# Optimization experiments

Measured on AMD Instinct MI355X. Metric: run time of the kernel, lower is better.

Reference implementation:

```python
import jax, jax.numpy as jnp
import numpy as np
from jax import lax

B, L, D, C = 4096, 50, 128, 64
V = 100000
H = D // 2  # bidirectional LSTM hidden size; 2*H == emb_dim


def setup_inputs() -> dict:
    key = jax.random.key(0)
    ks = jax.random.split(key, 26)
    f = lambda k, s: jax.random.normal(k, s, dtype=jnp.float32) * 0.05
    return {
        "r_idx": jax.random.randint(ks[0], (B,), 0, V),
        "a_idx": jax.random.randint(ks[1], (B,), 0, V),
        "acc_idx": jax.random.randint(ks[2], (B,), 0, V),
        "rank_q": jax.random.normal(ks[3], (B, L, D), dtype=jnp.float32),
        "rank_q_len": jax.random.randint(ks[4], (B,), 0, L),
        "ru_emb": f(ks[5], (V, D)),
        "au_emb": f(ks[6], (V, D)),
        "Wih_f": f(ks[7], (4 * H, D)), "Whh_f": f(ks[8], (4 * H, H)),
        "bih_f": f(ks[9], (4 * H,)), "bhh_f": f(ks[10], (4 * H,)),
        "Wih_b": f(ks[11], (4 * H, D)), "Whh_b": f(ks[12], (4 * H, H)),
        "bih_b": f(ks[13], (4 * H,)), "bhh_b": f(ks[14], (4 * H,)),
        "conv1_w": f(ks[15], (C, 1, D)), "conv1_b": f(ks[16], (C,)),
        "conv2_w": f(ks[17], (C, 2, D)), "conv2_b": f(ks[18], (C,)),
        "conv3_w": f(ks[19], (C, 3, D)), "conv3_b": f(ks[20], (C,)),
        "fc1_w": f(ks[21], (6,)), "fc1_b": f(ks[22], (1,)),
        "fc2_w": f(ks[23], (C,)), "fc2_b": f(ks[24], (1,)),
    }


def _lstm_dir(x, Wih, Whh, bih, bhh, reverse):
    # x: [B, L, D] -> outputs [B, L, H]; PyTorch gate order i,f,g,o
    b = x.shape[0]
    xs = jnp.swapaxes(x, 0, 1)  # [L, B, D]
    h0 = jnp.zeros((b, Whh.shape[1]), x.dtype)

    def step(carry, xt):
        h, c = carry
        gates = xt @ Wih.T + h @ Whh.T + (bih + bhh)
        i, fg, g, o = jnp.split(gates, 4, axis=-1)
        i = jax.nn.sigmoid(i)
        fg = jax.nn.sigmoid(fg)
        g = jnp.tanh(g)
        o = jax.nn.sigmoid(o)
        c = fg * c + i * g
        h = o * jnp.tanh(c)
        return (h, c), h

    _, ys = lax.scan(step, (h0, h0), xs, reverse=reverse)
    return jnp.swapaxes(ys, 0, 1)


def _score(mat, conv1_w, conv1_b, conv2_w, conv2_b, conv3_w, conv3_b, fc1_w, fc1_b, fc2_w, fc2_b):
    # mat: [B, 3, D]; three tiny conv branches (kernel heights 1/2/3, width=D)
    branches = []
    for w, bias in ((conv1_w, conv1_b), (conv2_w, conv2_b), (conv3_w, conv3_b)):
        k = w.shape[1]
        wins = jnp.stack([mat[:, i:i + k] for i in range(3 - k + 1)], axis=1)  # [B, W, k, D]
        branches.append(jax.nn.relu(jnp.einsum('bwkd,ckd->bcw', wins, w) + bias[None, :, None]))
    s = jnp.concatenate(branches, axis=2)  # [B, C, 6]
    h = jnp.einsum('bcw,w->bc', s, fc1_w) + fc1_b[0]  # fc_new_1: 6 -> 1
    return jnp.einsum('bc,c->b', h, fc2_w) + fc2_b[0]  # fc_new_2: C -> 1


def reference(r_idx, a_idx, acc_idx, rank_q, rank_q_len, ru_emb, au_emb,
              Wih_f, Whh_f, bih_f, bhh_f, Wih_b, Whh_b, bih_b, bhh_b,
              conv1_w, conv1_b, conv2_w, conv2_b, conv3_w, conv3_b,
              fc1_w, fc1_b, fc2_w, fc2_b):
    emb_r = ru_emb[r_idx]
    emb_a = au_emb[a_idx]
    emb_acc = au_emb[acc_idx]
    # bidirectional LSTM over the question sequence
    out_f = _lstm_dir(rank_q, Wih_f, Whh_f, bih_f, bhh_f, reverse=False)
    out_b = _lstm_dir(rank_q, Wih_b, Whh_b, bih_b, bhh_b, reverse=True)
    q_out = jnp.concatenate([out_f, out_b], axis=-1)  # [B, L, D]
    # prepend a zero timestep, then gather per-example at index rank_q_len
    q_pad = jnp.concatenate([jnp.zeros((q_out.shape[0], 1, q_out.shape[2]), q_out.dtype), q_out], axis=1)
    emb_q = q_pad[jnp.arange(q_pad.shape[0]), rank_q_len]  # [B, D]
    low = jnp.stack([emb_r, emb_q, emb_a], axis=1)   # [B, 3, D]
    high = jnp.stack([emb_r, emb_q, emb_acc], axis=1)
    fcp = (conv1_w, conv1_b, conv2_w, conv2_b, conv3_w, conv3_b, fc1_w, fc1_b, fc2_w, fc2_b)
    low_s = _score(low, *fcp)
    high_s = _score(high, *fcp)
    return jnp.sum(low_s - high_s)
```

## Files before the change

kernel.cpp:

```cpp
#include <hip/hip_runtime.h>
#include <hip/hip_bf16.h>

#define LSEQ 50
#define BATCH 4096

typedef __attribute__((ext_vector_type(8))) short bf16x8;
typedef __attribute__((ext_vector_type(4))) float f32x4;

__device__ __forceinline__ unsigned cvtpk(float lo, float hi) {
    unsigned r;
    asm("v_cvt_pk_bf16_f32 %0, %1, %2" : "=v"(r) : "v"(lo), "v"(hi));
    return r;
}
__device__ __forceinline__ bf16x8 pack8(float4 a, float4 b) {
    uint4 u;
    u.x = cvtpk(a.x, a.y); u.y = cvtpk(a.z, a.w);
    u.z = cvtpk(b.x, b.y); u.w = cvtpk(b.z, b.w);
    return __builtin_bit_cast(bf16x8, u);
}
__device__ __forceinline__ float fsigm(float x) {
    return __builtin_amdgcn_rcpf(1.0f + __builtin_amdgcn_exp2f(-1.44269504f * x));
}
__device__ __forceinline__ float ftanh(float x) {
    float e = __builtin_amdgcn_exp2f(2.88539008f * x);
    return 1.0f - 2.0f * __builtin_amdgcn_rcpf(e + 1.0f);
}

__global__ __launch_bounds__(256)
void sort_kernel(const int* __restrict__ qlen, int* __restrict__ perm)
{
    __shared__ int base[64];
    const int tid = threadIdx.x;
    if (tid < 64) base[tid] = 0;
    __syncthreads();
    for (int i = tid; i < BATCH; i += 256) atomicAdd(&base[qlen[i]], 1);
    __syncthreads();
    if (tid == 0) {
        int s = 0;
        for (int v = 0; v < 50; ++v) { int c = base[v]; base[v] = s; s += c; }
    }
    __syncthreads();
    for (int i = tid; i < BATCH; i += 256) {
        int pos = atomicAdd(&base[qlen[i]], 1);
        perm[pos] = i;
    }
}

__global__ __launch_bounds__(256, 2)
void lstm_kernel(const float* __restrict__ rank_q, const int* __restrict__ qlen,
                 const int* __restrict__ perm,
                 const float* __restrict__ Wih_f, const float* __restrict__ Whh_f,
                 const float* __restrict__ bih_f, const float* __restrict__ bhh_f,
                 const float* __restrict__ Wih_b, const float* __restrict__ Whh_b,
                 const float* __restrict__ bih_b, const float* __restrict__ bhh_b,
                 float* __restrict__ embq)
{
    const int blk = blockIdx.x;
    const int dir = blk >> 8;
    const int bb  = blk & 255;
    const int grp = (bb & 1) ? (255 - (bb >> 1)) : (bb >> 1);
    const int b0  = grp << 4;
    const int tid = threadIdx.x;
    const int wv  = tid >> 6;
    const int ln  = tid & 63;
    const int lm  = ln & 15;
    const int lq  = ln >> 4;
    const int m   = (wv << 4) + lm;

    const float* Wih = dir ? Wih_b : Wih_f;
    const float* Whh = dir ? Whh_b : Whh_f;
    const float* bih = dir ? bih_b : bih_f;
    const float* bhh = dir ? bhh_b : bhh_f;

    __shared__ __align__(16) unsigned short xbuf[3][16][136];
    __shared__ __align__(16) unsigned short hbuf[2][16][72];
    __shared__ int len_s[16];

    if (tid < 16) len_s[tid] = qlen[perm[b0 + tid]];
    for (int i = tid; i < 16 * 72; i += 256) ((unsigned short*)hbuf)[i] = 0;

    bf16x8 bfrag[4][6];
    float bias[4];
    #pragma unroll
    for (int j = 0; j < 4; ++j) {
        const int n = (j << 6) + m;
        bias[j] = bih[n] + bhh[n];
        #pragma unroll
        for (int s = 0; s < 6; ++s) {
            const int kb = (s << 5) + (lq << 3);
            const float* src = (s < 4) ? (Wih + n * 128 + kb)
                                       : (Whh + n * 64 + (kb - 128));
            bfrag[j][s] = pack8(*(const float4*)src, *(const float4*)(src + 4));
        }
    }

    int exq[4], len_e[4];
    #pragma unroll
    for (int r = 0; r < 4; ++r) {
        exq[r]   = perm[b0 + (lq << 2) + r];
        len_e[r] = qlen[exq[r]];
    }

    float cst[4]  = {0.f, 0.f, 0.f, 0.f};
    float qval[4] = {0.f, 0.f, 0.f, 0.f};

    const int se  = tid >> 4;
    const int exs = perm[b0 + se];
    const int sd  = (tid & 15) << 3;
    const int tstep = dir ? -128 : 128;
    const float* gp = rank_q + ((size_t)exs * LSEQ + (dir ? LSEQ - 1 : 0)) * 128 + sd;

    __syncthreads();

    int steps;
    if (dir == 0) {
        int mx = 0;
        #pragma unroll
        for (int i = 0; i < 16; ++i) mx = max(mx, len_s[i]);
        steps = mx;
    } else {
        int mn = 51;
        #pragma unroll
        for (int i = 0; i < 16; ++i) { int l = len_s[i]; mn = min(mn, l ? l : 51); }
        steps = (mn == 51) ? 0 : 51 - mn;
    }

    if (steps > 0) {
        {
            float4 a0 = *(const float4*)gp, b0v = *(const float4*)(gp + 4); gp += tstep;
            float4 a1 = *(const float4*)gp, b1v = *(const float4*)(gp + 4); gp += tstep;
            *(bf16x8*)&xbuf[0][se][sd] = pack8(a0, b0v);
            *(bf16x8*)&xbuf[1][se][sd] = pack8(a1, b1v);
        }
        float4 ha, hb2;
        if (3 <= steps) { ha = *(const float4*)gp; hb2 = *(const float4*)(gp + 4); gp += tstep; }
        __syncthreads();

        const int xoff = lm * 136 + (lq << 3);
        const int hoff = lm * 72 + (lq << 3);

        f32x4 accx[4];
        {
            const unsigned short* xb = &xbuf[0][0][0];
            bf16x8 x0 = *(const bf16x8*)(xb + xoff);
            bf16x8 x1 = *(const bf16x8*)(xb + xoff + 32);
            bf16x8 x2 = *(const bf16x8*)(xb + xoff + 64);
            bf16x8 x3 = *(const bf16x8*)(xb + xoff + 96);
            #pragma unroll
            for (int j = 0; j < 4; ++j) {
                f32x4 a = {bias[j], bias[j], bias[j], bias[j]};
                a = __builtin_amdgcn_mfma_f32_16x16x32_bf16(x0, bfrag[j][0], a, 0, 0, 0);
                a = __builtin_amdgcn_mfma_f32_16x16x32_bf16(x1, bfrag[j][1], a, 0, 0, 0);
                a = __builtin_amdgcn_mfma_f32_16x16x32_bf16(x2, bfrag[j][2], a, 0, 0, 0);
                a = __builtin_amdgcn_mfma_f32_16x16x32_bf16(x3, bfrag[j][3], a, 0, 0, 0);
                accx[j] = a;
            }
        }

        int r1 = 1, w2 = 2;
        for (int it = 0; it < steps; ++it) {
            const int t   = dir ? (LSEQ - 1 - it) : it;
            const int rbh = it & 1;
            const int wbh = rbh ^ 1;

            float4 na, nb;
            const bool nv = (it + 4 <= steps);
            if (nv) { na = *(const float4*)gp; nb = *(const float4*)(gp + 4); gp += tstep; }

            const unsigned short* hb = &hbuf[rbh][0][0];
            bf16x8 ah0 = *(const bf16x8*)(hb + hoff);
            bf16x8 ah1 = *(const bf16x8*)(hb + hoff + 32);
            f32x4 gate[4];
            #pragma unroll
            for (int j = 0; j < 4; ++j) {
                f32x4 a = __builtin_amdgcn_mfma_f32_16x16x32_bf16(ah0, bfrag[j][4], accx[j], 0, 0, 0);
                gate[j]  = __builtin_amdgcn_mfma_f32_16x16x32_bf16(ah1, bfrag[j][5], a, 0, 0, 0);
            }

            if (it + 1 < steps) {
                const unsigned short* xb = &xbuf[r1][0][0];
                bf16x8 x0 = *(const bf16x8*)(xb + xoff);
                bf16x8 x1 = *(const bf16x8*)(xb + xoff + 32);
                bf16x8 x2 = *(const bf16x8*)(xb + xoff + 64);
                bf16x8 x3 = *(const bf16x8*)(xb + xoff + 96);
                #pragma unroll
                for (int j = 0; j < 4; ++j) {
                    f32x4 a = {bias[j], bias[j], bias[j], bias[j]};
                    a = __builtin_amdgcn_mfma_f32_16x16x32_bf16(x0, bfrag[j][0], a, 0, 0, 0);
                    a = __builtin_amdgcn_mfma_f32_16x16x32_bf16(x1, bfrag[j][1], a, 0, 0, 0);
                    a = __builtin_amdgcn_mfma_f32_16x16x32_bf16(x2, bfrag[j][2], a, 0, 0, 0);
                    a = __builtin_amdgcn_mfma_f32_16x16x32_bf16(x3, bfrag[j][3], a, 0, 0, 0);
                    accx[j] = a;
                }
            }

            float hn[4];
            #pragma unroll
            for (int r = 0; r < 4; ++r) {
                float ig = fsigm(gate[0][r]);
                float fg = fsigm(gate[1][r]);
                float gg = ftanh(gate[2][r]);
                float og = fsigm(gate[3][r]);
                float cn = fg * cst[r] + ig * gg;
                cst[r] = cn;
                hn[r] = og * ftanh(cn);
                if (t == len_e[r] - 1) qval[r] = hn[r];
            }
            const unsigned u01 = cvtpk(hn[0], hn[1]);
            const unsigned u23 = cvtpk(hn[2], hn[3]);
            hbuf[wbh][(lq << 2) + 0][m] = (unsigned short)u01;
            hbuf[wbh][(lq << 2) + 1][m] = (unsigned short)(u01 >> 16);
            hbuf[wbh][(lq << 2) + 2][m] = (unsigned short)u23;
            hbuf[wbh][(lq << 2) + 3][m] = (unsigned short)(u23 >> 16);

            if (it + 3 <= steps) *(bf16x8*)&xbuf[w2][se][sd] = pack8(ha, hb2);
            ha = na; hb2 = nb;

            __syncthreads();
            r1 = (r1 == 2) ? 0 : r1 + 1;
            w2 = (w2 == 2) ? 0 : w2 + 1;
        }
    }

    #pragma unroll
    for (int r = 0; r < 4; ++r)
        embq[(size_t)exq[r] * 128 + (dir << 6) + m] = qval[r];
}

__global__ __launch_bounds__(256)
void prep_kernel(const float* __restrict__ c1w, const float* __restrict__ c2w,
                 const float* __restrict__ c3w, float* __restrict__ T)
{
    const int id = blockIdx.x * 256 + threadIdx.x;
    const int m  = id >> 13;
    const int rem = id & 8191;
    const int j  = rem >> 8;
    const int q  = rem & 255;
    const int c  = q >> 2;
    const int d  = (j << 2) + (q & 3);
    const float* src;
    switch (m) {
        case 0:  src = c1w + c * 128 + d;       break;
        case 1:  src = c2w + c * 256 + d;       break;
        case 2:  src = c2w + c * 256 + 128 + d; break;
        case 3:  src = c3w + c * 384 + d;       break;
        case 4:  src = c3w + c * 384 + 128 + d; break;
        default: src = c3w + c * 384 + 256 + d; break;
    }
    T[id] = *src;
}

__global__ __launch_bounds__(256)
void score_kernel(const int* __restrict__ r_idx, const int* __restrict__ a_idx,
                  const int* __restrict__ acc_idx,
                  const float* __restrict__ ru, const float* __restrict__ au,
                  const float* __restrict__ embq, const float* __restrict__ T,
                  const float* __restrict__ c1b, const float* __restrict__ c2b,
                  const float* __restrict__ c3b,
                  const float* __restrict__ fc1w, const float* __restrict__ fc2w,
                  float* __restrict__ diff)
{
    const int tid = threadIdx.x;
    const int wv  = tid >> 6;
    const int c   = tid & 63;
    const int b0  = blockIdx.x << 4;

    __shared__ __align__(16) float emb[64][132];
    {
        const int row = tid & 63;
        const int e   = row >> 2, v = row & 3;
        const int seg = (tid >> 6) << 5;
        const int bb  = b0 + e;
        const float* src = (v == 0) ? ru   + (size_t)r_idx[bb]   * 128 :
                           (v == 1) ? embq + (size_t)bb          * 128 :
                           (v == 2) ? au   + (size_t)a_idx[bb]   * 128 :
                                      au   + (size_t)acc_idx[bb] * 128;
        #pragma unroll
        for (int i = 0; i < 8; ++i) {
            float4 x = *(const float4*)(src + seg + (i << 2));
            *(float4*)&emb[row][seg + (i << 2)] = x;
        }
    }
    __syncthreads();

    float acc[4][9];
    #pragma unroll
    for (int e = 0; e < 4; ++e)
        #pragma unroll
        for (int k = 0; k < 9; ++k) acc[e][k] = 0.f;

    const float4* Tq = (const float4*)T;
    for (int j = 0; j < 32; ++j) {
        const float4* wq = Tq + j * 64 + c;
        const float4 w1  = wq[0];
        const float4 w20 = wq[2048];
        const float4 w21 = wq[4096];
        const float4 w30 = wq[6144];
        const float4 w31 = wq[8192];
        const float4 w32 = wq[10240];
        const int jd = j << 2;
        #pragma unroll
        for (int e = 0; e < 4; ++e) {
            const int br = ((wv << 2) + e) << 2;
            const float4 er = *(const float4*)&emb[br + 0][jd];
            const float4 eq = *(const float4*)&emb[br + 1][jd];
            const float4 ea = *(const float4*)&emb[br + 2][jd];
            const float4 ex = *(const float4*)&emb[br + 3][jd];
            acc[e][0] += w1.x*ea.x  + w1.y*ea.y  + w1.z*ea.z  + w1.w*ea.w;
            acc[e][1] += w1.x*ex.x  + w1.y*ex.y  + w1.z*ex.z  + w1.w*ex.w;
            acc[e][2] += w20.x*eq.x + w20.y*eq.y + w20.z*eq.z + w20.w*eq.w;
            acc[e][3] += w21.x*ea.x + w21.y*ea.y + w21.z*ea.z + w21.w*ea.w;
            acc[e][4] += w21.x*ex.x + w21.y*ex.y + w21.z*ex.z + w21.w*ex.w;
            acc[e][5] += w30.x*er.x + w30.y*er.y + w30.z*er.z + w30.w*er.w;
            acc[e][6] += w31.x*eq.x + w31.y*eq.y + w31.z*eq.z + w31.w*eq.w;
            acc[e][7] += w32.x*ea.x + w32.y*ea.y + w32.z*ea.z + w32.w*ea.w;
            acc[e][8] += w32.x*ex.x + w32.y*ex.y + w32.z*ex.z + w32.w*ex.w;
        }
    }

    const float b1 = c1b[c], b2 = c2b[c], b3 = c3b[c], f2 = fc2w[c];
    const float f12 = fc1w[2], f14 = fc1w[4], f15 = fc1w[5];
    #pragma unroll
    for (int e = 0; e < 4; ++e) {
        const float r1 = fmaxf(acc[e][0] + b1, 0.f) - fmaxf(acc[e][1] + b1, 0.f);
        const float r2 = fmaxf(acc[e][2] + acc[e][3] + b2, 0.f)
                       - fmaxf(acc[e][2] + acc[e][4] + b2, 0.f);
        const float r3 = fmaxf(acc[e][5] + acc[e][6] + acc[e][7] + b3, 0.f)
                       - fmaxf(acc[e][5] + acc[e][6] + acc[e][8] + b3, 0.f);
        float term = f2 * (f12 * r1 + f14 * r2 + f15 * r3);
        #pragma unroll
        for (int off = 32; off; off >>= 1) term += __shfl_down(term, off);
        if (c == 0) diff[b0 + (wv << 2) + e] = term;
    }
}

__global__ void reduce_kernel(const float* __restrict__ diff, float* __restrict__ out)
{
    __shared__ float s[256];
    const int tid = threadIdx.x;
    float v = 0.f;
    for (int i = tid; i < BATCH; i += 256) v += diff[i];
    s[tid] = v;
    __syncthreads();
    for (int st = 128; st > 0; st >>= 1) {
        if (tid < st) s[tid] += s[tid + st];
        __syncthreads();
    }
    if (tid == 0) out[0] = s[0];
}

extern "C" void kernel_launch(void* const* d_in, const int* in_sizes, int n_in,
                              void* d_out, int out_size, void* d_ws, size_t ws_size,
                              hipStream_t stream) {
    (void)in_sizes; (void)n_in; (void)out_size; (void)ws_size;
    const int*   r_idx   = (const int*)d_in[0];
    const int*   a_idx   = (const int*)d_in[1];
    const int*   acc_idx = (const int*)d_in[2];
    const float* rank_q  = (const float*)d_in[3];
    const int*   qlen    = (const int*)d_in[4];
    const float* ru      = (const float*)d_in[5];
    const float* au      = (const float*)d_in[6];
    const float* Wih_f   = (const float*)d_in[7];
    const float* Whh_f   = (const float*)d_in[8];
    const float* bih_f   = (const float*)d_in[9];
    const float* bhh_f   = (const float*)d_in[10];
    const float* Wih_b   = (const float*)d_in[11];
    const float* Whh_b   = (const float*)d_in[12];
    const float* bih_b   = (const float*)d_in[13];
    const float* bhh_b   = (const float*)d_in[14];
    const float* c1w     = (const float*)d_in[15];
    const float* c1b     = (const float*)d_in[16];
    const float* c2w     = (const float*)d_in[17];
    const float* c2b     = (const float*)d_in[18];
    const float* c3w     = (const float*)d_in[19];
    const float* c3b     = (const float*)d_in[20];
    const float* fc1w    = (const float*)d_in[21];
    const float* fc2w    = (const float*)d_in[23];

    float* embq = (float*)d_ws;
    float* diff = embq + (size_t)BATCH * 128;
    float* T    = diff + BATCH;
    int*   perm = (int*)(T + 49152);

    sort_kernel<<<1, 256, 0, stream>>>(qlen, perm);
    prep_kernel<<<192, 256, 0, stream>>>(c1w, c2w, c3w, T);
    lstm_kernel<<<512, 256, 0, stream>>>(rank_q, qlen, perm,
                                         Wih_f, Whh_f, bih_f, bhh_f,
                                         Wih_b, Whh_b, bih_b, bhh_b, embq);
    score_kernel<<<BATCH / 16, 256, 0, stream>>>(r_idx, a_idx, acc_idx, ru, au, embq, T,
                                                 c1b, c2b, c3b, fc1w, fc2w, diff);
    reduce_kernel<<<1, 256, 0, stream>>>(diff, (float*)d_out);
}
```

Before: 95.26 us.

## Fuse forward and backward LSTM directions into one 512-thread block

Each block now runs the forward direction for one length-sorted group in its first half and the backward direction for the mirrored group in its second half, with separate shared buffers per half. Both halves iterate to the larger of their step counts and share barriers, with inactive halves skipping work. The pairing aims to balance per-block work and halve the block count, at the cost of wider barriers, idle waves in the shorter half, and tighter register limits from the larger launch bound.

```diff
diff --git a/kernel.cpp b/kernel.cpp
--- a/kernel.cpp
+++ b/kernel.cpp
@@ -46,7 +46,7 @@
     }
 }
 
-__global__ __launch_bounds__(256, 2)
+__global__ __launch_bounds__(512, 2)
 void lstm_kernel(const float* __restrict__ rank_q, const int* __restrict__ qlen,
                  const int* __restrict__ perm,
                  const float* __restrict__ Wih_f, const float* __restrict__ Whh_f,
@@ -55,29 +55,31 @@
                  const float* __restrict__ bih_b, const float* __restrict__ bhh_b,
                  float* __restrict__ embq)
 {
-    const int blk = blockIdx.x;
-    const int dir = blk >> 8;
-    const int bb  = blk & 255;
-    const int grp = (bb & 1) ? (255 - (bb >> 1)) : (bb >> 1);
-    const int b0  = grp << 4;
-    const int tid = threadIdx.x;
-    const int wv  = tid >> 6;
-    const int ln  = tid & 63;
-    const int lm  = ln & 15;
-    const int lq  = ln >> 4;
-    const int m   = (wv << 4) + lm;
+    const int blk  = blockIdx.x;
+    const int tid  = threadIdx.x;
+    const int half = tid >> 8;
+    const int htid = tid & 255;
+    const int dir  = half;
+    const int grp  = half ? (255 - blk) : blk;
+    const int b0   = grp << 4;
+    const int wv   = htid >> 6;
+    const int ln   = htid & 63;
+    const int lm   = ln & 15;
+    const int lq   = ln >> 4;
+    const int m    = (wv << 4) + lm;
 
     const float* Wih = dir ? Wih_b : Wih_f;
     const float* Whh = dir ? Whh_b : Whh_f;
     const float* bih = dir ? bih_b : bih_f;
     const float* bhh = dir ? bhh_b : bhh_f;
 
-    __shared__ __align__(16) unsigned short xbuf[3][16][136];
-    __shared__ __align__(16) unsigned short hbuf[2][16][72];
-    __shared__ int len_s[16];
-
-    if (tid < 16) len_s[tid] = qlen[perm[b0 + tid]];
-    for (int i = tid; i < 16 * 72; i += 256) ((unsigned short*)hbuf)[i] = 0;
+    __shared__ __align__(16) unsigned short xbuf[2][3][16][136];
+    __shared__ __align__(16) unsigned short hbuf[2][2][16][72];
+    __shared__ int len_sh[2][16];
+    __shared__ int steps_sh[2];
+
+    if (htid < 16) len_sh[half][htid] = qlen[perm[b0 + htid]];
+    for (int i = htid; i < 16 * 72; i += 256) ((unsigned short*)hbuf[half])[i] = 0;
 
     bf16x8 bfrag[4][6];
     float bias[4];
@@ -104,9 +106,9 @@
     float cst[4]  = {0.f, 0.f, 0.f, 0.f};
     float qval[4] = {0.f, 0.f, 0.f, 0.f};
 
-    const int se  = tid >> 4;
+    const int se  = htid >> 4;
     const int exs = perm[b0 + se];
-    const int sd  = (tid & 15) << 3;
+    const int sd  = (htid & 15) << 3;
     const int tstep = dir ? -128 : 128;
     const float* gp = rank_q + ((size_t)exs * LSEQ + (dir ? LSEQ - 1 : 0)) * 128 + sd;
 
@@ -116,58 +118,60 @@
     if (dir == 0) {
         int mx = 0;
         #pragma unroll
-        for (int i = 0; i < 16; ++i) mx = max(mx, len_s[i]);
+        for (int i = 0; i < 16; ++i) mx = max(mx, len_sh[0][i]);
         steps = mx;
     } else {
         int mn = 51;
         #pragma unroll
-        for (int i = 0; i < 16; ++i) { int l = len_s[i]; mn = min(mn, l ? l : 51); }
+        for (int i = 0; i < 16; ++i) { int l = len_sh[1][i]; mn = min(mn, l ? l : 51); }
         steps = (mn == 51) ? 0 : 51 - mn;
     }
-
+    if (htid == 0) steps_sh[half] = steps;
+    __syncthreads();
+    const int smax = max(steps_sh[0], steps_sh[1]);
+
+    const int xoff = lm * 136 + (lq << 3);
+    const int hoff = lm * 72 + (lq << 3);
+
+    float4 ha, hb2;
     if (steps > 0) {
-        {
-            float4 a0 = *(const float4*)gp, b0v = *(const float4*)(gp + 4); gp += tstep;
-            float4 a1 = *(const float4*)gp, b1v = *(const float4*)(gp + 4); gp += tstep;
-            *(bf16x8*)&xbuf[0][se][sd] = pack8(a0, b0v);
-            *(bf16x8*)&xbuf[1][se][sd] = pack8(a1, b1v);
-        }
-        float4 ha, hb2;
+        float4 a0 = *(const float4*)gp, b0v = *(const float4*)(gp + 4); gp += tstep;
+        float4 a1 = *(const float4*)gp, b1v = *(const float4*)(gp + 4); gp += tstep;
+        *(bf16x8*)&xbuf[half][0][se][sd] = pack8(a0, b0v);
+        *(bf16x8*)&xbuf[half][1][se][sd] = pack8(a1, b1v);
         if (3 <= steps) { ha = *(const float4*)gp; hb2 = *(const float4*)(gp + 4); gp += tstep; }
-        __syncthreads();
-
-        const int xoff = lm * 136 + (lq << 3);
-        const int hoff = lm * 72 + (lq << 3);
-
-        f32x4 accx[4];
-        {
-            const unsigned short* xb = &xbuf[0][0][0];
-            bf16x8 x0 = *(const bf16x8*)(xb + xoff);
-            bf16x8 x1 = *(const bf16x8*)(xb + xoff + 32);
-            bf16x8 x2 = *(const bf16x8*)(xb + xoff + 64);
-            bf16x8 x3 = *(const bf16x8*)(xb + xoff + 96);
-            #pragma unroll
-            for (int j = 0; j < 4; ++j) {
-                f32x4 a = {bias[j], bias[j], bias[j], bias[j]};
-                a = __builtin_amdgcn_mfma_f32_16x16x32_bf16(x0, bfrag[j][0], a, 0, 0, 0);
-                a = __builtin_amdgcn_mfma_f32_16x16x32_bf16(x1, bfrag[j][1], a, 0, 0, 0);
-                a = __builtin_amdgcn_mfma_f32_16x16x32_bf16(x2, bfrag[j][2], a, 0, 0, 0);
-                a = __builtin_amdgcn_mfma_f32_16x16x32_bf16(x3, bfrag[j][3], a, 0, 0, 0);
-                accx[j] = a;
-            }
-        }
-
-        int r1 = 1, w2 = 2;
-        for (int it = 0; it < steps; ++it) {
+    }
+    __syncthreads();
+
+    f32x4 accx[4];
+    if (steps > 0) {
+        const unsigned short* xb = &xbuf[half][0][0][0];
+        bf16x8 x0 = *(const bf16x8*)(xb + xoff);
+        bf16x8 x1 = *(const bf16x8*)(xb + xoff + 32);
+        bf16x8 x2 = *(const bf16x8*)(xb + xoff + 64);
+        bf16x8 x3 = *(const bf16x8*)(xb + xoff + 96);
+        #pragma unroll
+        for (int j = 0; j < 4; ++j) {
+            f32x4 a = {bias[j], bias[j], bias[j], bias[j]};
+            a = __builtin_amdgcn_mfma_f32_16x16x32_bf16(x0, bfrag[j][0], a, 0, 0, 0);
+            a = __builtin_amdgcn_mfma_f32_16x16x32_bf16(x1, bfrag[j][1], a, 0, 0, 0);
+            a = __builtin_amdgcn_mfma_f32_16x16x32_bf16(x2, bfrag[j][2], a, 0, 0, 0);
+            a = __builtin_amdgcn_mfma_f32_16x16x32_bf16(x3, bfrag[j][3], a, 0, 0, 0);
+            accx[j] = a;
+        }
+    }
+
+    int r1 = 1, w2 = 2;
+    for (int it = 0; it < smax; ++it) {
+        if (it < steps) {
             const int t   = dir ? (LSEQ - 1 - it) : it;
             const int rbh = it & 1;
             const int wbh = rbh ^ 1;
 
             float4 na, nb;
-            const bool nv = (it + 4 <= steps);
-            if (nv) { na = *(const float4*)gp; nb = *(const float4*)(gp + 4); gp += tstep; }
-
-            const unsigned short* hb = &hbuf[rbh][0][0];
+            if (it + 4 <= steps) { na = *(const float4*)gp; nb = *(const float4*)(gp + 4); gp += tstep; }
+
+            const unsigned short* hb = &hbuf[half][rbh][0][0];
             bf16x8 ah0 = *(const bf16x8*)(hb + hoff);
             bf16x8 ah1 = *(const bf16x8*)(hb + hoff + 32);
             f32x4 gate[4];
@@ -178,7 +182,7 @@
             }
 
             if (it + 1 < steps) {
-                const unsigned short* xb = &xbuf[r1][0][0];
+                const unsigned short* xb = &xbuf[half][r1][0][0];
                 bf16x8 x0 = *(const bf16x8*)(xb + xoff);
                 bf16x8 x1 = *(const bf16x8*)(xb + xoff + 32);
                 bf16x8 x2 = *(const bf16x8*)(xb + xoff + 64);
@@ -208,18 +212,17 @@
             }
             const unsigned u01 = cvtpk(hn[0], hn[1]);
             const unsigned u23 = cvtpk(hn[2], hn[3]);
-            hbuf[wbh][(lq << 2) + 0][m] = (unsigned short)u01;
-            hbuf[wbh][(lq << 2) + 1][m] = (unsigned short)(u01 >> 16);
-            hbuf[wbh][(lq << 2) + 2][m] = (unsigned short)u23;
-            hbuf[wbh][(lq << 2) + 3][m] = (unsigned short)(u23 >> 16);
-
-            if (it + 3 <= steps) *(bf16x8*)&xbuf[w2][se][sd] = pack8(ha, hb2);
+            hbuf[half][wbh][(lq << 2) + 0][m] = (unsigned short)u01;
+            hbuf[half][wbh][(lq << 2) + 1][m] = (unsigned short)(u01 >> 16);
+            hbuf[half][wbh][(lq << 2) + 2][m] = (unsigned short)u23;
+            hbuf[half][wbh][(lq << 2) + 3][m] = (unsigned short)(u23 >> 16);
+
+            if (it + 3 <= steps) *(bf16x8*)&xbuf[half][w2][se][sd] = pack8(ha, hb2);
             ha = na; hb2 = nb;
-
-            __syncthreads();
-            r1 = (r1 == 2) ? 0 : r1 + 1;
-            w2 = (w2 == 2) ? 0 : w2 + 1;
-        }
+        }
+        __syncthreads();
+        r1 = (r1 == 2) ? 0 : r1 + 1;
+        w2 = (w2 == 2) ? 0 : w2 + 1;
     }
 
     #pragma unroll
@@ -384,7 +387,7 @@
 
     sort_kernel<<<1, 256, 0, stream>>>(qlen, perm);
     prep_kernel<<<192, 256, 0, stream>>>(c1w, c2w, c3w, T);
-    lstm_kernel<<<512, 256, 0, stream>>>(rank_q, qlen, perm,
+    lstm_kernel<<<256, 512, 0, stream>>>(rank_q, qlen, perm,
                                          Wih_f, Whh_f, bih_f, bhh_f,
                                          Wih_b, Whh_b, bih_b, bhh_b, embq);
     score_kernel<<<BATCH / 16, 256, 0, stream>>>(r_idx, a_idx, acc_idx, ru, au, embq, T,
```

New measurement: 114.4 us. 20.1% more time.

## Halve LSTM batch tile to 8 examples per block and double grid size

Applied to the files above, without the earlier changes.

Each LSTM block now handles 8 sorted examples instead of 16, launching 1024 blocks with forward/backward directions interleaved and ordered so long and short sequences mix. The MFMA tile stays 16 rows, so the upper half is zero-padded and half the lanes skip the activation math. Smaller groups let each block's step count track its own max/min length more tightly and spread work over more CUs. The cost is half-wasted MFMA throughput and twice the weight-fragment loading. The __syncthreads is also replaced with an explicit lgkmcnt wait plus s_barrier.

```diff
diff --git a/kernel.cpp b/kernel.cpp
--- a/kernel.cpp
+++ b/kernel.cpp
@@ -56,10 +56,10 @@
                  float* __restrict__ embq)
 {
     const int blk = blockIdx.x;
-    const int dir = blk >> 8;
-    const int bb  = blk & 255;
-    const int grp = (bb & 1) ? (255 - (bb >> 1)) : (bb >> 1);
-    const int b0  = grp << 4;
+    const int dir = blk & 1;
+    const int g   = blk >> 1;
+    const int grp = dir ? g : (511 - g);
+    const int b0  = grp << 3;
     const int tid = threadIdx.x;
     const int wv  = tid >> 6;
     const int ln  = tid & 63;
@@ -74,10 +74,11 @@
 
     __shared__ __align__(16) unsigned short xbuf[3][16][136];
     __shared__ __align__(16) unsigned short hbuf[2][16][72];
-    __shared__ int len_s[16];
-
-    if (tid < 16) len_s[tid] = qlen[perm[b0 + tid]];
-    for (int i = tid; i < 16 * 72; i += 256) ((unsigned short*)hbuf)[i] = 0;
+    __shared__ int len_sh[8];
+
+    if (tid < 8) len_sh[tid] = qlen[perm[b0 + tid]];
+    for (int i = tid; i < 3 * 16 * 136; i += 256) ((unsigned short*)xbuf)[i] = 0;
+    for (int i = tid; i < 2 * 16 * 72;  i += 256) ((unsigned short*)hbuf)[i] = 0;
 
     bf16x8 bfrag[4][6];
     float bias[4];
@@ -97,16 +98,16 @@
     int exq[4], len_e[4];
     #pragma unroll
     for (int r = 0; r < 4; ++r) {
-        exq[r]   = perm[b0 + (lq << 2) + r];
-        len_e[r] = qlen[exq[r]];
+        if (lq < 2) { exq[r] = perm[b0 + (lq << 2) + r]; len_e[r] = qlen[exq[r]]; }
+        else        { exq[r] = 0; len_e[r] = -1000; }
     }
 
     float cst[4]  = {0.f, 0.f, 0.f, 0.f};
     float qval[4] = {0.f, 0.f, 0.f, 0.f};
 
     const int se  = tid >> 4;
-    const int exs = perm[b0 + se];
     const int sd  = (tid & 15) << 3;
+    const int exs = (se < 8) ? perm[b0 + se] : 0;
     const int tstep = dir ? -128 : 128;
     const float* gp = rank_q + ((size_t)exs * LSEQ + (dir ? LSEQ - 1 : 0)) * 128 + sd;
 
@@ -116,32 +117,69 @@
     if (dir == 0) {
         int mx = 0;
         #pragma unroll
-        for (int i = 0; i < 16; ++i) mx = max(mx, len_s[i]);
+        for (int i = 0; i < 8; ++i) mx = max(mx, len_sh[i]);
         steps = mx;
     } else {
         int mn = 51;
         #pragma unroll
-        for (int i = 0; i < 16; ++i) { int l = len_s[i]; mn = min(mn, l ? l : 51); }
+        for (int i = 0; i < 8; ++i) { int l = len_sh[i]; mn = min(mn, l ? l : 51); }
         steps = (mn == 51) ? 0 : 51 - mn;
     }
 
+    float4 ha, hb2;
+    if (steps > 0 && se < 8) {
+        float4 a0 = *(const float4*)gp, b0v = *(const float4*)(gp + 4); gp += tstep;
+        float4 a1 = *(const float4*)gp, b1v = *(const float4*)(gp + 4); gp += tstep;
+        *(bf16x8*)&xbuf[0][se][sd] = pack8(a0, b0v);
+        *(bf16x8*)&xbuf[1][se][sd] = pack8(a1, b1v);
+        if (3 <= steps) { ha = *(const float4*)gp; hb2 = *(const float4*)(gp + 4); gp += tstep; }
+    }
+    __syncthreads();
+
+    const int xoff = lm * 136 + (lq << 3);
+    const int hoff = lm * 72 + (lq << 3);
+
+    f32x4 accx[4];
     if (steps > 0) {
-        {
-            float4 a0 = *(const float4*)gp, b0v = *(const float4*)(gp + 4); gp += tstep;
-            float4 a1 = *(const float4*)gp, b1v = *(const float4*)(gp + 4); gp += tstep;
-            *(bf16x8*)&xbuf[0][se][sd] = pack8(a0, b0v);
-            *(bf16x8*)&xbuf[1][se][sd] = pack8(a1, b1v);
-        }
-        float4 ha, hb2;
-        if (3 <= steps) { ha = *(const float4*)gp; hb2 = *(const float4*)(gp + 4); gp += tstep; }
-        __syncthreads();
-
-        const int xoff = lm * 136 + (lq << 3);
-        const int hoff = lm * 72 + (lq << 3);
-
-        f32x4 accx[4];
-        {
-            const unsigned short* xb = &xbuf[0][0][0];
+        const unsigned short* xb = &xbuf[0][0][0];
+        bf16x8 x0 = *(const bf16x8*)(xb + xoff);
+        bf16x8 x1 = *(const bf16x8*)(xb + xoff + 32);
+        bf16x8 x2 = *(const bf16x8*)(xb + xoff + 64);
+        bf16x8 x3 = *(const bf16x8*)(xb + xoff + 96);
+        #pragma unroll
+        for (int j = 0; j < 4; ++j) {
+            f32x4 a = {bias[j], bias[j], bias[j], bias[j]};
+            a = __builtin_amdgcn_mfma_f32_16x16x32_bf16(x0, bfrag[j][0], a, 0, 0, 0);
+            a = __builtin_amdgcn_mfma_f32_16x16x32_bf16(x1, bfrag[j][1], a, 0, 0, 0);
+            a = __builtin_amdgcn_mfma_f32_16x16x32_bf16(x2, bfrag[j][2], a, 0, 0, 0);
+            a = __builtin_amdgcn_mfma_f32_16x16x32_bf16(x3, bfrag[j][3], a, 0, 0, 0);
+            accx[j] = a;
+        }
+    }
+
+    int r1 = 1, w2 = 2;
+    for (int it = 0; it < steps; ++it) {
+        const int t   = dir ? (LSEQ - 1 - it) : it;
+        const int rbh = it & 1;
+        const int wbh = rbh ^ 1;
+
+        float4 na, nb;
+        if (se < 8 && it + 4 <= steps) {
+            na = *(const float4*)gp; nb = *(const float4*)(gp + 4); gp += tstep;
+        }
+
+        const unsigned short* hb = &hbuf[rbh][0][0];
+        bf16x8 ah0 = *(const bf16x8*)(hb + hoff);
+        bf16x8 ah1 = *(const bf16x8*)(hb + hoff + 32);
+        f32x4 gate[4];
+        #pragma unroll
+        for (int j = 0; j < 4; ++j) {
+            f32x4 a = __builtin_amdgcn_mfma_f32_16x16x32_bf16(ah0, bfrag[j][4], accx[j], 0, 0, 0);
+            gate[j]  = __builtin_amdgcn_mfma_f32_16x16x32_bf16(ah1, bfrag[j][5], a, 0, 0, 0);
+        }
+
+        if (it + 1 < steps) {
+            const unsigned short* xb = &xbuf[r1][0][0];
             bf16x8 x0 = *(const bf16x8*)(xb + xoff);
             bf16x8 x1 = *(const bf16x8*)(xb + xoff + 32);
             bf16x8 x2 = *(const bf16x8*)(xb + xoff + 64);
@@ -157,43 +195,7 @@
             }
         }
 
-        int r1 = 1, w2 = 2;
-        for (int it = 0; it < steps; ++it) {
-            const int t   = dir ? (LSEQ - 1 - it) : it;
-            const int rbh = it & 1;
-            const int wbh = rbh ^ 1;
-
-            float4 na, nb;
-            const bool nv = (it + 4 <= steps);
-            if (nv) { na = *(const float4*)gp; nb = *(const float4*)(gp + 4); gp += tstep; }
-
-            const unsigned short* hb = &hbuf[rbh][0][0];
-            bf16x8 ah0 = *(const bf16x8*)(hb + hoff);
-            bf16x8 ah1 = *(const bf16x8*)(hb + hoff + 32);
-            f32x4 gate[4];
-            #pragma unroll
-            for (int j = 0; j < 4; ++j) {
-                f32x4 a = __builtin_amdgcn_mfma_f32_16x16x32_bf16(ah0, bfrag[j][4], accx[j], 0, 0, 0);
-                gate[j]  = __builtin_amdgcn_mfma_f32_16x16x32_bf16(ah1, bfrag[j][5], a, 0, 0, 0);
-            }
-
-            if (it + 1 < steps) {
-                const unsigned short* xb = &xbuf[r1][0][0];
-                bf16x8 x0 = *(const bf16x8*)(xb + xoff);
-                bf16x8 x1 = *(const bf16x8*)(xb + xoff + 32);
-                bf16x8 x2 = *(const bf16x8*)(xb + xoff + 64);
-                bf16x8 x3 = *(const bf16x8*)(xb + xoff + 96);
-                #pragma unroll
-                for (int j = 0; j < 4; ++j) {
-                    f32x4 a = {bias[j], bias[j], bias[j], bias[j]};
-                    a = __builtin_amdgcn_mfma_f32_16x16x32_bf16(x0, bfrag[j][0], a, 0, 0, 0);
-                    a = __builtin_amdgcn_mfma_f32_16x16x32_bf16(x1, bfrag[j][1], a, 0, 0, 0);
-                    a = __builtin_amdgcn_mfma_f32_16x16x32_bf16(x2, bfrag[j][2], a, 0, 0, 0);
-                    a = __builtin_amdgcn_mfma_f32_16x16x32_bf16(x3, bfrag[j][3], a, 0, 0, 0);
-                    accx[j] = a;
-                }
-            }
-
+        if (lq < 2) {
             float hn[4];
             #pragma unroll
             for (int r = 0; r < 4; ++r) {
@@ -212,19 +214,25 @@
             hbuf[wbh][(lq << 2) + 1][m] = (unsigned short)(u01 >> 16);
             hbuf[wbh][(lq << 2) + 2][m] = (unsigned short)u23;
             hbuf[wbh][(lq << 2) + 3][m] = (unsigned short)(u23 >> 16);
-
-            if (it + 3 <= steps) *(bf16x8*)&xbuf[w2][se][sd] = pack8(ha, hb2);
-            ha = na; hb2 = nb;
-
-            __syncthreads();
-            r1 = (r1 == 2) ? 0 : r1 + 1;
-            w2 = (w2 == 2) ? 0 : w2 + 1;
-        }
-    }
-
-    #pragma unroll
-    for (int r = 0; r < 4; ++r)
-        embq[(size_t)exq[r] * 128 + (dir << 6) + m] = qval[r];
+        }
+
+        if (se < 8 && it + 3 <= steps) *(bf16x8*)&xbuf[w2][se][sd] = pack8(ha, hb2);
+        ha = na; hb2 = nb;
+
+        __builtin_amdgcn_sched_barrier(0);
+        asm volatile("s_waitcnt lgkmcnt(0)" ::: "memory");
+        __builtin_amdgcn_s_barrier();
+        __builtin_amdgcn_sched_barrier(0);
+
+        r1 = (r1 == 2) ? 0 : r1 + 1;
+        w2 = (w2 == 2) ? 0 : w2 + 1;
+    }
+
+    if (lq < 2) {
+        #pragma unroll
+        for (int r = 0; r < 4; ++r)
+            embq[(size_t)exq[r] * 128 + (dir << 6) + m] = qval[r];
+    }
 }
 
 __global__ __launch_bounds__(256)
@@ -384,9 +392,9 @@
 
     sort_kernel<<<1, 256, 0, stream>>>(qlen, perm);
     prep_kernel<<<192, 256, 0, stream>>>(c1w, c2w, c3w, T);
-    lstm_kernel<<<512, 256, 0, stream>>>(rank_q, qlen, perm,
-                                         Wih_f, Whh_f, bih_f, bhh_f,
-                                         Wih_b, Whh_b, bih_b, bhh_b, embq);
+    lstm_kernel<<<1024, 256, 0, stream>>>(rank_q, qlen, perm,
+                                          Wih_f, Whh_f, bih_f, bhh_f,
+                                          Wih_b, Whh_b, bih_b, bhh_b, embq);
     score_kernel<<<BATCH / 16, 256, 0, stream>>>(r_idx, a_idx, acc_idx, ru, au, embq, T,
                                                  c1b, c2b, c3b, fc1w, fc2w, diff);
     reduce_kernel<<<1, 256, 0, stream>>>(diff, (float*)d_out);
```

New measurement: 116.8 us. 1.23x slower.
